# Performance work log

Hardware: AMD Instinct MI355X
Metric: run time of the kernel (lower is better)

Reference implementation:

```python
import jax, jax.numpy as jnp
import numpy as np

T, I, H, F = 4096, 512, 2048, 256

def setup_inputs() -> dict:
    key = jax.random.key(0)
    ks = jax.random.split(key, 16)
    s = lambda i, shape: jax.random.normal(ks[i], shape, dtype=jnp.float32) * 0.02
    sequence = jax.random.normal(ks[0], (1, T, I), dtype=jnp.float32)
    mask = (jax.random.uniform(ks[1], (1, T, I)) < 0.8).astype(jnp.float32)
    delta = jax.random.uniform(ks[2], (1, T, I), dtype=jnp.float32)
    dt = jax.random.uniform(ks[3], (1, T), minval=0.1, maxval=1.0, dtype=jnp.float32)
    h0 = jax.random.normal(ks[4], (1, H), dtype=jnp.float32)
    dh0 = jax.random.normal(ks[5], (1, H), dtype=jnp.float32)
    prex0 = jnp.zeros((1, I), jnp.float32)
    return dict(
        sequence=sequence, mask=mask, delta=delta, dt=dt,
        h0=h0, dh0=dh0, prex0=prex0,
        Wgx=s(6, (I, I)), bgx=jnp.zeros((I,), jnp.float32),
        Wgh=s(7, (I, H)), bgh=jnp.zeros((H,), jnp.float32),
        W=s(8, (I, 3 * H)), U=s(9, (H, 3 * H)), V=s(10, (I, 3 * H)), b=jnp.zeros((3 * H,), jnp.float32),
        We=s(11, (H, F)), be=jnp.zeros((F,), jnp.float32),
        Wd=s(12, (F, H)), bd=jnp.zeros((H,), jnp.float32),
        Wo=s(13, (H, I)), bo=jnp.zeros((I,), jnp.float32),
    )

def reference(sequence, mask, delta, dt, h0, dh0, prex0,
              Wgx, bgx, Wgh, bgh, W, U, V, b, We, be, Wd, bd, Wo, bo):
    Hd = h0.shape[-1]
    # GRU-D style empirical mean over observed steps: (1, I)
    mean = jnp.sum(sequence, 1) / (1e-6 + jnp.sum(mask != 0, 1))

    def cell(h, prex, x, m, d):
        # decay gates from time-gap d
        gx = jnp.exp(-jax.nn.relu(d @ Wgx + bgx))          # (1, I)
        gh = jnp.exp(-jax.nn.relu(d @ Wgh + bgh))          # (1, H)
        xh = m * x + (1.0 - m) * (gx * prex + (1.0 - gx) * mean)
        hd = gh * h
        pre = xh @ W + m @ V + b                           # (1, 3H)
        zr = jax.nn.sigmoid(pre[:, :2 * Hd] + hd @ U[:, :2 * Hd])
        z, r = zr[:, :Hd], zr[:, Hd:]
        htil = jnp.tanh(pre[:, 2 * Hd:] + (r * hd) @ U[:, 2 * Hd:])
        h_post = z * hd + (1.0 - z) * htil
        dh = (1.0 - z) * (htil - hd)                       # GRU-TV time derivative
        return h_post, dh, xh

    seq_t = jnp.swapaxes(sequence, 0, 1)  # (T, 1, I)
    msk_t = jnp.swapaxes(mask, 0, 1)
    dlt_t = jnp.swapaxes(delta, 0, 1)
    dts = dt[0]                            # (T,)

    def enc_step(c, xs):
        h, dh, prex = c
        x, m, d, t = xs
        h_post, dh, prex = cell(h, prex, x, m, d)
        return (h + t * dh, dh, prex), h_post

    (h, dh, prex), hps = jax.lax.scan(enc_step, (h0, dh0, prex0), (seq_t, msk_t, dlt_t, dts))
    h_post = jax.nn.relu(hps[-1])
    feature = jax.nn.relu(h_post @ We + be)
    h = feature @ Wd + bd

    Tn = seq_t.shape[0]
    layer = Tn - 1  # dt > 0 everywhere, so the break never triggers
    rev = lambda a: a[:layer][::-1]

    def dec_step(c, xs):
        h, dh, prex = c
        x, m, d, t = xs
        h_post, dh, prex = cell(h, prex, x, m, d)
        return (h + t * dh, dh, prex), h_post @ Wo + bo

    _, outs = jax.lax.scan(dec_step, (h, dh, prex), (rev(seq_t), rev(msk_t), rev(dlt_t), rev(dts)))
    out_sequence = outs[::-1, 0, :]  # (T-1, I), matches torch.cat of reversed list
    return out_sequence
```

## Files before the change

kernel.cpp:

```cpp
#include <hip/hip_runtime.h>
#include <cmath>

#define NSTEP 8191
#define POLL_MAX 32768
#define RESC_MAX 8192
#define ARR_SPIN (1 << 14)

typedef unsigned long long u64;

__device__ __forceinline__ unsigned tagOf(u64 v){ return (unsigned)(v >> 32); }
__device__ __forceinline__ void pubTag(u64* p, unsigned e, float x){
  atomicExch(p, ((u64)e << 32) | (u64)(unsigned)__float_as_int(x));
}
__device__ __forceinline__ void pubMark(u64* p, unsigned e){
  atomicExch(p, ((u64)e << 32));
}
__device__ __forceinline__ float lo32f(u64 v){ return __int_as_float((int)(unsigned)v); }

__device__ __forceinline__ int pollMark(u64* p, unsigned e){
  int spin = 0;
  for(;;){
    u64 v = ((spin & 7) == 7) ? atomicOr(p, 0ull)
          : __hip_atomic_load(p, __ATOMIC_RELAXED, __HIP_MEMORY_SCOPE_AGENT);
    if (tagOf(v) >= e) return 1;
    if (++spin >= POLL_MAX) return 0;
    __builtin_amdgcn_s_sleep(1);
  }
}
__device__ __forceinline__ int loadPay8(u64* base, int idx, unsigned e, u64 out[8]){
  #pragma unroll
  for (int i = 0; i < 8; ++i)
    out[i] = __hip_atomic_load(base + i*256 + idx, __ATOMIC_RELAXED,
                               __HIP_MEMORY_SCOPE_AGENT);
  unsigned mn = 0xFFFFFFFFu;
  #pragma unroll
  for (int i = 0; i < 8; ++i){ unsigned tg = tagOf(out[i]); mn = tg < mn ? tg : mn; }
  if (mn >= e) return 1;
  int spin = 0;
  for(;;){
    #pragma unroll
    for (int i = 0; i < 8; ++i)
      if (tagOf(out[i]) < e) out[i] = atomicOr(base + i*256 + idx, 0ull);
    mn = 0xFFFFFFFFu;
    #pragma unroll
    for (int i = 0; i < 8; ++i){ unsigned tg = tagOf(out[i]); mn = tg < mn ? tg : mn; }
    if (mn >= e) return 1;
    if (++spin >= RESC_MAX) return 0;
    __builtin_amdgcn_s_sleep(1);
  }
}
__device__ __forceinline__ int poll1p(u64* p, unsigned e, u64* out){
  int spin = 0;
  for(;;){
    u64 v = ((spin & 7) == 7) ? atomicOr(p, 0ull)
          : __hip_atomic_load(p, __ATOMIC_RELAXED, __HIP_MEMORY_SCOPE_AGENT);
    if (tagOf(v) >= e){ *out = v; return 1; }
    if (++spin >= POLL_MAX) return 0;
    __builtin_amdgcn_s_sleep(1);
  }
}

__global__ void fillK(float* p, int n, float v){
  for (int i = blockIdx.x*blockDim.x + threadIdx.x; i < n; i += gridDim.x*blockDim.x) p[i] = v;
}

__global__ void initK(u64* pub, int* ctrl, const float* __restrict__ h0){
  int t = threadIdx.x;
  #pragma unroll
  for (int i = 0; i < 8; ++i)
    pub[i*256 + t] = (u64)(unsigned)__float_as_int(h0[8*t + i]);
  for (int j = 2048 + t; j < 6656; j += 256) pub[j] = 0;
  for (int i = t; i < 1024; i += 256) ctrl[i] = 0;
}

__global__ void mean1K(const float* __restrict__ seq, const float* __restrict__ mask,
                       float* __restrict__ Sp, float* __restrict__ Cp){
  int bb = blockIdx.x, i = threadIdx.x;
  float s = 0.f, c = 0.f;
  for (int tt = 64*bb; tt < 64*bb + 64; ++tt){
    size_t o = (size_t)tt*512 + i;
    s += seq[o];
    c += (mask[o] != 0.f) ? 1.f : 0.f;
  }
  Sp[bb*512 + i] = s; Cp[bb*512 + i] = c;
}
__global__ void mean2K(const float* __restrict__ Sp, const float* __restrict__ Cp,
                       float* __restrict__ meanv){
  int i = threadIdx.x;
  float s = 0.f, c = 0.f;
  for (int bb = 0; bb < 64; ++bb){ s += Sp[bb*512 + i]; c += Cp[bb*512 + i]; }
  meanv[i] = s / (1e-6f + c);
}

__device__ __forceinline__ void scan_ac(const float* __restrict__ Gx,
                                        const float* __restrict__ mask,
                                        const float* __restrict__ seq,
                                        float mn, int r, int i, float& a, float& c){
  int src = (r < 4096) ? r : (8190 - r);
  size_t o = (size_t)src*512 + i;
  float g = Gx[o], m = mask[o], x = seq[o];
  a = (1.f - m)*g;
  c = m*x + (1.f - m)*(1.f - g)*mn;
}
__global__ void scanSegK(const float* __restrict__ Gx, const float* __restrict__ mask,
                         const float* __restrict__ seq, const float* __restrict__ meanv,
                         float* __restrict__ segA, float* __restrict__ segC){
  int bb = blockIdx.x, i = threadIdx.x;
  float mn = meanv[i];
  float A = 1.f, C = 0.f;
  int r1 = 128*bb + 128; if (r1 > NSTEP) r1 = NSTEP;
  for (int r = 128*bb; r < r1; ++r){
    float a, c; scan_ac(Gx, mask, seq, mn, r, i, a, c);
    A = a*A; C = a*C + c;
  }
  segA[bb*512 + i] = A; segC[bb*512 + i] = C;
}
__global__ void scanFixK(const float* __restrict__ segA, const float* __restrict__ segC,
                         const float* __restrict__ prex0, float* __restrict__ segX0){
  int i = threadIdx.x;
  float x = prex0[i];
  for (int bb = 0; bb < 64; ++bb){
    segX0[bb*512 + i] = x;
    x = segA[bb*512 + i]*x + segC[bb*512 + i];
  }
}
__global__ void scanEmitK(const float* __restrict__ Gx, const float* __restrict__ mask,
                          const float* __restrict__ seq, const float* __restrict__ meanv,
                          const float* __restrict__ segX0, float* __restrict__ xh){
  int bb = blockIdx.x, i = threadIdx.x;
  float mn = meanv[i];
  float x = segX0[bb*512 + i];
  int r1 = 128*bb + 128; if (r1 > NSTEP) r1 = NSTEP;
  for (int r = 128*bb; r < r1; ++r){
    float a, c; scan_ac(Gx, mask, seq, mn, r, i, a, c);
    x = a*x + c;
    xh[(size_t)r*512 + i] = x;
  }
}

#define BM 128
#define BN 128
#define BK 8
__launch_bounds__(256)
__global__ void gemmK(const float* __restrict__ A, const float* __restrict__ B,
                      float* __restrict__ C, int M, int N, int K,
                      const float* __restrict__ bias, int act, int beta, int amap,
                      int rowoff){
  __shared__ float As[BK][BM+4];
  __shared__ float Bs[BK][BN+4];
  int tid = threadIdx.x;
  int r0 = blockIdx.y * BM, c0 = blockIdx.x * BN;
  int tr = tid >> 4, tc = tid & 15;
  int ar = tid >> 1, ak = (tid & 1)*4;
  int bkr = tid >> 5, bkc = (tid & 31)*4;
  float acc[2][2][4][4] = {};

  for (int k0 = 0; k0 < K; k0 += BK){
    int r = r0 + ar;
    float4 av = make_float4(0.f,0.f,0.f,0.f);
    if (r < M){
      int g = rowoff + r;
      int rs = amap ? (g < 4096 ? g : 8190 - g) : r;
      av = *(const float4*)(A + (size_t)rs*K + k0 + ak);
    }
    As[ak+0][ar] = av.x; As[ak+1][ar] = av.y; As[ak+2][ar] = av.z; As[ak+3][ar] = av.w;
    *(float4*)(&Bs[bkr][bkc]) = *(const float4*)(B + (size_t)(k0 + bkr)*N + c0 + bkc);
    __syncthreads();
    #pragma unroll
    for (int kk = 0; kk < BK; ++kk){
      float4 a0 = *(const float4*)(&As[kk][tr*4]);
      float4 a1 = *(const float4*)(&As[kk][64 + tr*4]);
      float4 b0 = *(const float4*)(&Bs[kk][tc*4]);
      float4 b1 = *(const float4*)(&Bs[kk][64 + tc*4]);
      float avr[2][4] = {{a0.x,a0.y,a0.z,a0.w},{a1.x,a1.y,a1.z,a1.w}};
      float bvr[2][4] = {{b0.x,b0.y,b0.z,b0.w},{b1.x,b1.y,b1.z,b1.w}};
      #pragma unroll
      for (int ri = 0; ri < 2; ++ri)
        #pragma unroll
        for (int ci = 0; ci < 2; ++ci)
          #pragma unroll
          for (int ii = 0; ii < 4; ++ii)
            #pragma unroll
            for (int jj = 0; jj < 4; ++jj)
              acc[ri][ci][ii][jj] += avr[ri][ii]*bvr[ci][jj];
    }
    __syncthreads();
  }

  #pragma unroll
  for (int ri = 0; ri < 2; ++ri)
    #pragma unroll
    for (int ii = 0; ii < 4; ++ii){
      int r = r0 + ri*64 + tr*4 + ii;
      if (r >= M) continue;
      #pragma unroll
      for (int ci = 0; ci < 2; ++ci){
        int cbase = c0 + ci*64 + tc*4;
        float v[4];
        #pragma unroll
        for (int jj = 0; jj < 4; ++jj){
          float x = acc[ri][ci][ii][jj];
          if (bias) x += bias[cbase + jj];
          if (act == 1) x = expf(-fmaxf(x, 0.f));
          v[jj] = x;
        }
        float* cp = C + (size_t)r*N + cbase;
        if (beta){
          float4 o = *(const float4*)cp;
          v[0]+=o.x; v[1]+=o.y; v[2]+=o.z; v[3]+=o.w;
        }
        *(float4*)cp = make_float4(v[0],v[1],v[2],v[3]);
      }
    }
}

__launch_bounds__(256, 1)
__global__ void rnnPersK(const float* __restrict__ U, const float* __restrict__ PreC,
                         int c0, int len, int ev0,
                         const float* __restrict__ Gh, const float* __restrict__ dts,
                         const float* __restrict__ We, const float* __restrict__ be,
                         const float* __restrict__ Wd, const float* __restrict__ bd,
                         u64* pub, float* __restrict__ HpDec, int* arrival){
  const int w = blockIdx.x;
  const int t = threadIdx.x;
  const int lane = t & 63, wv = t >> 6;
  __shared__ float redA[4][8], redB[4][8], redH[4][8], ldsH[8], ldsHd[8];
  __shared__ int okArr;

  u64* hP   = pub;
  u64* rhdP = pub + 2048;
  u64* hpP  = pub + 4096;
  u64* feat = pub + 6144;
  u64* mark = pub + 6400;

  if (t == 0){
    atomicAdd(arrival, 1);
    int ok = 1, spin = 0;
    while (atomicOr(arrival, 0) < 256){
      if (++spin >= ARR_SPIN){ ok = 0; break; }
      __builtin_amdgcn_s_sleep(2);
    }
    okArr = ok;
  }
  __syncthreads();
  if (!okArr){ if (t == 0) HpDec[w] = 77777.f; return; }

  float uz[8][8], ur[8][8], uh[8][8];
  #pragma unroll
  for (int i = 0; i < 8; ++i){
    const float* row = U + (size_t)(8*t + i)*6144 + 8*w;
    #pragma unroll
    for (int cc = 0; cc < 8; ++cc){
      uz[cc][i] = row[cc];
      ur[cc][i] = row[2048 + cc];
      uh[cc][i] = row[4096 + cc];
    }
  }

  unsigned e = (unsigned)ev0;

  float ghn[8]; float pzn = 0.f, prn = 0.f, phn = 0.f, dtn = 0.f;
  auto prefetch = [&](int g){
    int src = (g < 4096) ? g : (8190 - g);
    const float* gr = Gh + (size_t)src*2048 + 8*t;
    #pragma unroll
    for (int i = 0; i < 8; ++i) ghn[i] = gr[i];
    const float* prow = PreC + (size_t)(g - c0)*6144;
    if (t < 8){ pzn = prow[8*w + t]; phn = prow[4096 + 8*w + t]; dtn = dts[src]; }
    else if (t < 16){ prn = prow[2048 + 8*w + (t - 8)]; }
  };
  prefetch(c0);

  for (int sl = 0; sl < len; ++sl){
    int g = c0 + sl;

    if (g == 4096){
      {
        int okM = pollMark(mark + t, e);
        u64 hpw[8];
        int okP = okM ? loadPay8(hpP, t, e, hpw) : 0;
        if (__syncthreads_or(!okP)) goto bail;
        float part = 0.f;
        #pragma unroll
        for (int i = 0; i < 8; ++i)
          part += fmaxf(lo32f(hpw[i]), 0.f) * We[(size_t)(8*t + i)*256 + w];
        #pragma unroll
        for (int o = 32; o; o >>= 1) part += __shfl_down(part, o);
        if (lane == 0) redA[wv][0] = part;
        __syncthreads();
        if (t == 0)
          pubTag(feat + w, e + 1,
                 fmaxf(redA[0][0]+redA[1][0]+redA[2][0]+redA[3][0] + be[w], 0.f));
      }
      {
        u64 fw;
        int okF = poll1p(feat + t, e + 1, &fw);
        if (__syncthreads_or(!okF)) goto bail;
        float fv = lo32f(fw);
        #pragma unroll
        for (int cc = 0; cc < 8; ++cc){
          float v2 = fv * Wd[(size_t)t*2048 + 8*w + cc];
          #pragma unroll
          for (int o = 32; o; o >>= 1) v2 += __shfl_down(v2, o);
          if (lane == 0) redB[wv][cc] = v2;
        }
        __syncthreads();
        if (t < 8)
          pubTag(hP + t*256 + w, e + 2,
                 redB[0][t]+redB[1][t]+redB[2][t]+redB[3][t] + bd[8*w + t]);
        __syncthreads();
        if (t == 0) pubMark(mark + w, e + 2);
      }
      e += 2;
    }

    {
      float ghc[8];
      #pragma unroll
      for (int i = 0; i < 8; ++i) ghc[i] = ghn[i];
      float pz = pzn, pr = prn, ph = phn, dtv = dtn;

      int okA = pollMark(mark + t, e);
      u64 hw[8];
      int okP = okA ? loadPay8(hP, t, e, hw) : 0;
      float hv[8], hd[8];
      #pragma unroll
      for (int i = 0; i < 8; ++i){
        hv[i] = lo32f(hw[i]);
        hd[i] = hv[i] * ghc[i];
      }
      if (t == w){
        #pragma unroll
        for (int i = 0; i < 8; ++i){ ldsH[i] = hv[i]; ldsHd[i] = hd[i]; }
      }
      if (__syncthreads_or(!okP)) goto bail;
      if (sl + 1 < len) prefetch(g + 1);

      float accz[8], accr[8];
      #pragma unroll
      for (int cc = 0; cc < 8; ++cc){
        float az = 0.f, ar_ = 0.f;
        #pragma unroll
        for (int i = 0; i < 8; ++i){ az += hd[i]*uz[cc][i]; ar_ += hd[i]*ur[cc][i]; }
        accz[cc] = az; accr[cc] = ar_;
      }
      #pragma unroll
      for (int cc = 0; cc < 8; ++cc){
        float v = accz[cc];
        #pragma unroll
        for (int o = 32; o; o >>= 1) v += __shfl_down(v, o);
        if (lane == 0) redA[wv][cc] = v;
        v = accr[cc];
        #pragma unroll
        for (int o = 32; o; o >>= 1) v += __shfl_down(v, o);
        if (lane == 0) redB[wv][cc] = v;
      }
      __syncthreads();
      float zreg = 0.f;
      if (t < 8){
        float s = redA[0][t]+redA[1][t]+redA[2][t]+redA[3][t] + pz;
        zreg = 1.f/(1.f + expf(-s));
      } else if (t < 16){
        int cc = t - 8;
        float s = redB[0][cc]+redB[1][cc]+redB[2][cc]+redB[3][cc] + pr;
        float r = 1.f/(1.f + expf(-s));
        pubTag(rhdP + cc*256 + w, e + 1, r * ldsHd[cc]);
      }
      __syncthreads();
      if (t == 0) pubMark(mark + w, e + 1);

      int okB = pollMark(mark + t, e + 1);
      u64 rw[8];
      int okQ = okB ? loadPay8(rhdP, t, e + 1, rw) : 0;
      if (__syncthreads_or(!okQ)) goto bail;
      float rv[8];
      #pragma unroll
      for (int i = 0; i < 8; ++i) rv[i] = lo32f(rw[i]);

      float acch[8];
      #pragma unroll
      for (int cc = 0; cc < 8; ++cc){
        float a = 0.f;
        #pragma unroll
        for (int i = 0; i < 8; ++i) a += rv[i]*uh[cc][i];
        acch[cc] = a;
      }
      #pragma unroll
      for (int cc = 0; cc < 8; ++cc){
        float v = acch[cc];
        #pragma unroll
        for (int o = 32; o; o >>= 1) v += __shfl_down(v, o);
        if (lane == 0) redH[wv][cc] = v;
      }
      __syncthreads();
      if (t < 8){
        float u2   = redH[0][t]+redH[1][t]+redH[2][t]+redH[3][t] + ph;
        float htil = tanhf(u2);
        float z = zreg, hdv = ldsHd[t], hold = ldsH[t];
        float hp = z*hdv + (1.f - z)*htil;
        float dh = (1.f - z)*(htil - hdv);
        pubTag(hP + t*256 + w, e + 2, hold + dtv*dh);
        if (g == 4095) pubTag(hpP + t*256 + w, e + 2, hp);
        if (g >= 4096) HpDec[(size_t)(8190 - g)*2048 + 8*w + t] = hp;
      }
      __syncthreads();
      if (t == 0) pubMark(mark + w, e + 2);
      e += 2;
    }
  }
  return;

bail:
  if (t == 0) HpDec[w] = 77777.f;
}

extern "C" void kernel_launch(void* const* d_in, const int* in_sizes, int n_in,
                              void* d_out, int out_size, void* d_ws, size_t ws_size,
                              hipStream_t stream){
  (void)in_sizes; (void)n_in;
  const float* seq   = (const float*)d_in[0];
  const float* mask  = (const float*)d_in[1];
  const float* delta = (const float*)d_in[2];
  const float* dt    = (const float*)d_in[3];
  const float* h0    = (const float*)d_in[4];
  const float* prex0 = (const float*)d_in[6];
  const float* Wgx   = (const float*)d_in[7];
  const float* bgx   = (const float*)d_in[8];
  const float* Wgh   = (const float*)d_in[9];
  const float* bgh   = (const float*)d_in[10];
  const float* W     = (const float*)d_in[11];
  const float* U     = (const float*)d_in[12];
  const float* V     = (const float*)d_in[13];
  const float* b     = (const float*)d_in[14];
  const float* We    = (const float*)d_in[15];
  const float* be    = (const float*)d_in[16];
  const float* Wd    = (const float*)d_in[17];
  const float* bd    = (const float*)d_in[18];
  const float* Wo    = (const float*)d_in[19];
  const float* bo    = (const float*)d_in[20];

  float* wsf = (float*)d_ws;
  size_t wsFloats = ws_size / 4;
  size_t off = 0;
  u64*   pub    = (u64*)(wsf + off);  off += 13312;
  int*   ctrl   = (int*)(wsf + off);  off += 1024;
  float* meanv  = wsf + off;  off += 512;
  float* Sp     = wsf + off;  off += (size_t)64*512;
  float* Cp     = wsf + off;  off += (size_t)64*512;
  float* Gh     = wsf + off;  off += (size_t)4096*2048;
  float* xh_all = wsf + off;  off += (size_t)NSTEP*512;
  float* HpDec  = wsf + off;  off += (size_t)4095*2048;
  size_t fixedF = off;

  float* area  = wsf + fixedF;
  float* Gx    = area;
  float* segA  = area + (size_t)4096*512;
  float* segC  = segA + (size_t)64*512;
  float* segX0 = segC + (size_t)64*512;
  size_t preNeed = (size_t)4096*512 + (size_t)3*64*512;

  size_t areaF = (wsFloats > fixedF) ? (wsFloats - fixedF) : 0;
  long chunkSteps = (long)(areaF / 6144);
  if (areaF < preNeed || chunkSteps < 64){
    fillK<<<dim3(256), dim3(256), 0, stream>>>((float*)d_out, out_size,
                                               1.0e6f + (float)(ws_size >> 20));
    return;
  }
  if (chunkSteps > NSTEP) chunkSteps = NSTEP;
  int nch  = (int)((NSTEP + chunkSteps - 1) / chunkSteps);
  if (nch > 128) nch = 128;
  int clen = (NSTEP + nch - 1) / nch;

  mean1K<<<dim3(64), dim3(512), 0, stream>>>(seq, mask, Sp, Cp);
  mean2K<<<dim3(1),  dim3(512), 0, stream>>>(Sp, Cp, meanv);
  gemmK<<<dim3(4, 32),  dim3(256), 0, stream>>>(delta, Wgx, Gx, 4096, 512, 512, bgx, 1, 0, 0, 0);
  gemmK<<<dim3(16, 32), dim3(256), 0, stream>>>(delta, Wgh, Gh, 4096, 2048, 512, bgh, 1, 0, 0, 0);
  scanSegK<<<dim3(64), dim3(512), 0, stream>>>(Gx, mask, seq, meanv, segA, segC);
  scanFixK<<<dim3(1),  dim3(512), 0, stream>>>(segA, segC, prex0, segX0);
  scanEmitK<<<dim3(64), dim3(512), 0, stream>>>(Gx, mask, seq, meanv, segX0, xh_all);
  initK<<<dim3(1), dim3(256), 0, stream>>>(pub, ctrl, h0);

  int ev = 0, chunkIdx = 0;
  for (int c0 = 0; c0 < NSTEP; c0 += clen, ++chunkIdx){
    int len = (c0 + clen <= NSTEP) ? clen : (NSTEP - c0);
    int gy  = (len + 127) / 128;
    gemmK<<<dim3(48, gy), dim3(256), 0, stream>>>(xh_all + (size_t)c0*512, W, area,
                                                  len, 6144, 512, b, 0, 0, 0, 0);
    gemmK<<<dim3(48, gy), dim3(256), 0, stream>>>(mask, V, area,
                                                  len, 6144, 512, nullptr, 0, 1, 1, c0);

    rnnPersK<<<dim3(256), dim3(256), 0, stream>>>(U, area, c0, len, ev, Gh, dt,
                                                  We, be, Wd, bd,
                                                  pub, HpDec, ctrl + 4*chunkIdx);
    ev += 2*len + ((c0 <= 4096 && 4096 < c0 + len) ? 2 : 0);
  }

  gemmK<<<dim3(4, 32), dim3(256), 0, stream>>>(HpDec, Wo, (float*)d_out,
                                               4095, 512, 2048, bo, 0, 0, 0, 0);
}
```

Baseline: 112.5 ms.

## Fuse xh@W projection into persistent RNN kernel and drop chunked launches

Each persistent block now keeps its 24 columns of W in LDS and computes the xh@W input projection for the next step inside the recurrence, overlapping it with the wait for the r*hd exchange. The mask@V+b term is precomputed once for all 4096 source steps, so the per-chunk GEMM launches and the chunk loop are removed and a single persistent kernel runs all 8191 steps. This removes the large per-chunk preactivation buffer, its re-reads, and repeated kernel launches with their grid barriers. In exchange it adds per-step reductions and two extra __syncthreads to the serial critical path, and uses about 48 KB of LDS per block.

```diff
diff --git a/kernel.cpp b/kernel.cpp
--- a/kernel.cpp
+++ b/kernel.cpp
@@ -215,7 +215,8 @@
 }
 
 __launch_bounds__(256, 1)
-__global__ void rnnPersK(const float* __restrict__ U, const float* __restrict__ PreC,
+__global__ void rnnPersK(const float* __restrict__ U, const float* __restrict__ W,
+                         const float* __restrict__ MV, const float* __restrict__ xh_all,
                          int c0, int len, int ev0,
                          const float* __restrict__ Gh, const float* __restrict__ dts,
                          const float* __restrict__ We, const float* __restrict__ be,
@@ -225,6 +226,8 @@
   const int t = threadIdx.x;
   const int lane = t & 63, wv = t >> 6;
   __shared__ float redA[4][8], redB[4][8], redH[4][8], ldsH[8], ldsHd[8];
+  __shared__ float redP[4][24], preL[24];
+  __shared__ float W2[24][513];
   __shared__ int okArr;
 
   u64* hP   = pub;
@@ -256,20 +259,46 @@
       uh[cc][i] = row[4096 + cc];
     }
   }
+  for (int idx = t; idx < 24*512; idx += 256){
+    int c = idx >> 9, k = idx & 511;
+    int col = (c < 8) ? 8*w + c : (c < 16) ? 2048 + 8*w + (c-8) : 4096 + 8*w + (c-16);
+    W2[c][k] = W[(size_t)k*6144 + col];
+  }
+  __syncthreads();
 
   unsigned e = (unsigned)ev0;
 
-  float ghn[8]; float pzn = 0.f, prn = 0.f, phn = 0.f, dtn = 0.f;
+  float ghn[8];
   auto prefetch = [&](int g){
     int src = (g < 4096) ? g : (8190 - g);
     const float* gr = Gh + (size_t)src*2048 + 8*t;
     #pragma unroll
     for (int i = 0; i < 8; ++i) ghn[i] = gr[i];
-    const float* prow = PreC + (size_t)(g - c0)*6144;
-    if (t < 8){ pzn = prow[8*w + t]; phn = prow[4096 + 8*w + t]; dtn = dts[src]; }
-    else if (t < 16){ prn = prow[2048 + 8*w + (t - 8)]; }
+  };
+  auto computePre = [&](int g){
+    int src = (g < 4096) ? g : (8190 - g);
+    float2 xh2 = *(const float2*)(xh_all + (size_t)g*512 + 2*t);
+    float pacc[24];
+    #pragma unroll
+    for (int c = 0; c < 24; ++c)
+      pacc[c] = W2[c][2*t]*xh2.x + W2[c][2*t+1]*xh2.y;
+    #pragma unroll
+    for (int c = 0; c < 24; ++c){
+      float v = pacc[c];
+      #pragma unroll
+      for (int o = 32; o; o >>= 1) v += __shfl_down(v, o);
+      if (lane == 0) redP[wv][c] = v;
+    }
+    __syncthreads();
+    if (t < 24){
+      int col = (t < 8) ? 8*w + t : (t < 16) ? 2048 + 8*w + (t-8) : 4096 + 8*w + (t-16);
+      preL[t] = redP[0][t]+redP[1][t]+redP[2][t]+redP[3][t]
+              + MV[(size_t)src*6144 + col];
+    }
+    __syncthreads();
   };
   prefetch(c0);
+  computePre(c0);
 
   for (int sl = 0; sl < len; ++sl){
     int g = c0 + sl;
@@ -315,10 +344,15 @@
     }
 
     {
+      float pz = 0.f, pr = 0.f, ph = 0.f, dtv = 0.f;
+      {
+        int src = (g < 4096) ? g : (8190 - g);
+        if (t < 8){ pz = preL[t]; ph = preL[16 + t]; dtv = dts[src]; }
+        else if (t < 16){ pr = preL[t]; }
+      }
       float ghc[8];
       #pragma unroll
       for (int i = 0; i < 8; ++i) ghc[i] = ghn[i];
-      float pz = pzn, pr = prn, ph = phn, dtv = dtn;
 
       int okA = pollMark(mark + t, e);
       u64 hw[8];
@@ -368,6 +402,8 @@
       }
       __syncthreads();
       if (t == 0) pubMark(mark + w, e + 1);
+
+      if (sl + 1 < len) computePre(g + 1);
 
       int okB = pollMark(mark + t, e + 1);
       u64 rw[8];
@@ -450,50 +486,31 @@
   float* Gh     = wsf + off;  off += (size_t)4096*2048;
   float* xh_all = wsf + off;  off += (size_t)NSTEP*512;
   float* HpDec  = wsf + off;  off += (size_t)4095*2048;
-  size_t fixedF = off;
-
-  float* area  = wsf + fixedF;
-  float* Gx    = area;
-  float* segA  = area + (size_t)4096*512;
-  float* segC  = segA + (size_t)64*512;
-  float* segX0 = segC + (size_t)64*512;
-  size_t preNeed = (size_t)4096*512 + (size_t)3*64*512;
-
-  size_t areaF = (wsFloats > fixedF) ? (wsFloats - fixedF) : 0;
-  long chunkSteps = (long)(areaF / 6144);
-  if (areaF < preNeed || chunkSteps < 64){
+  float* MV     = wsf + off;  off += (size_t)4096*6144;
+  float* Gx     = wsf + off;  off += (size_t)4096*512;
+  float* segA   = wsf + off;  off += (size_t)64*512;
+  float* segC   = wsf + off;  off += (size_t)64*512;
+  float* segX0  = wsf + off;  off += (size_t)64*512;
+  size_t need = off;
+  if (wsFloats < need){
     fillK<<<dim3(256), dim3(256), 0, stream>>>((float*)d_out, out_size,
                                                1.0e6f + (float)(ws_size >> 20));
     return;
   }
-  if (chunkSteps > NSTEP) chunkSteps = NSTEP;
-  int nch  = (int)((NSTEP + chunkSteps - 1) / chunkSteps);
-  if (nch > 128) nch = 128;
-  int clen = (NSTEP + nch - 1) / nch;
 
   mean1K<<<dim3(64), dim3(512), 0, stream>>>(seq, mask, Sp, Cp);
   mean2K<<<dim3(1),  dim3(512), 0, stream>>>(Sp, Cp, meanv);
   gemmK<<<dim3(4, 32),  dim3(256), 0, stream>>>(delta, Wgx, Gx, 4096, 512, 512, bgx, 1, 0, 0, 0);
   gemmK<<<dim3(16, 32), dim3(256), 0, stream>>>(delta, Wgh, Gh, 4096, 2048, 512, bgh, 1, 0, 0, 0);
+  gemmK<<<dim3(48, 32), dim3(256), 0, stream>>>(mask, V, MV, 4096, 6144, 512, b, 0, 0, 0, 0);
   scanSegK<<<dim3(64), dim3(512), 0, stream>>>(Gx, mask, seq, meanv, segA, segC);
   scanFixK<<<dim3(1),  dim3(512), 0, stream>>>(segA, segC, prex0, segX0);
   scanEmitK<<<dim3(64), dim3(512), 0, stream>>>(Gx, mask, seq, meanv, segX0, xh_all);
   initK<<<dim3(1), dim3(256), 0, stream>>>(pub, ctrl, h0);
 
-  int ev = 0, chunkIdx = 0;
-  for (int c0 = 0; c0 < NSTEP; c0 += clen, ++chunkIdx){
-    int len = (c0 + clen <= NSTEP) ? clen : (NSTEP - c0);
-    int gy  = (len + 127) / 128;
-    gemmK<<<dim3(48, gy), dim3(256), 0, stream>>>(xh_all + (size_t)c0*512, W, area,
-                                                  len, 6144, 512, b, 0, 0, 0, 0);
-    gemmK<<<dim3(48, gy), dim3(256), 0, stream>>>(mask, V, area,
-                                                  len, 6144, 512, nullptr, 0, 1, 1, c0);
-
-    rnnPersK<<<dim3(256), dim3(256), 0, stream>>>(U, area, c0, len, ev, Gh, dt,
-                                                  We, be, Wd, bd,
-                                                  pub, HpDec, ctrl + 4*chunkIdx);
-    ev += 2*len + ((c0 <= 4096 && 4096 < c0 + len) ? 2 : 0);
-  }
+  rnnPersK<<<dim3(256), dim3(256), 0, stream>>>(U, W, MV, xh_all, 0, NSTEP, 0,
+                                                Gh, dt, We, be, Wd, bd,
+                                                pub, HpDec, ctrl);
 
   gemmK<<<dim3(4, 32), dim3(256), 0, stream>>>(HpDec, Wo, (float*)d_out,
                                                4095, 512, 2048, bo, 0, 0, 0, 0);
```

Result: slower. 138.8 ms (+23.4%).
